# Performance work log

Hardware: AMD Instinct MI355X
Metric: run time of the kernel (lower is better)

Reference implementation:

```python
import jax, jax.numpy as jnp
import numpy as np

B, OUT_LEN, IN_LEN, H = 8, 1024, 4096, 256


def setup_inputs() -> dict:
    key = jax.random.key(0)
    k1, k2, k3 = jax.random.split(key, 3)
    output = jax.random.normal(k1, (B, OUT_LEN, H), dtype=jnp.float32)
    encoder_outputs = jax.random.normal(k2, (B, IN_LEN, H), dtype=jnp.float32)
    # valid lengths in [1, IN_LEN] so every softmax row has >=1 unmasked entry
    lengths = jax.random.randint(k3, (B,), 1, IN_LEN + 1).astype(jnp.int32)
    return {"output": output, "encoder_outputs": encoder_outputs, "lengths": lengths}


def reference(output, encoder_outputs, lengths):
    # scores: [B, out_len, in_len], unscaled dot-product (as in the original)
    scores = jnp.einsum('boh,bih->boi', output, encoder_outputs)
    # mask[b, j] = j < lengths[b]; masked positions get -inf (additive mask)
    valid = jnp.arange(encoder_outputs.shape[1])[None, :] < lengths[:, None]  # [B, in_len]
    scores = jnp.where(valid[:, None, :], scores, -jnp.inf)
    attn = jax.nn.softmax(scores, axis=-1)  # [B, out_len, in_len]
    context = jnp.einsum('boi,bih->boh', attn, encoder_outputs)  # [B, out_len, H]
    return (context, attn)
```

## Files before the change

kernel.cpp:

```cpp
#include <hip/hip_runtime.h>
#include <hip/hip_bf16.h>
#include <math.h>

#define B_    8
#define OLEN  1024
#define ILEN  4096
#define HDIM  256
#define LDA   40
#define KSPLIT 4

typedef __attribute__((ext_vector_type(8))) short bf16x8;
typedef __attribute__((ext_vector_type(4))) float f32x4;

__device__ inline unsigned pk_bf16(float x, float y) {
  union { __hip_bfloat162 h; unsigned u; } c;
  c.h = __float22bfloat162_rn(make_float2(x, y));
  return c.u;
}
__device__ inline short f2bf(float x) {
  union { __hip_bfloat16 h; short s; } c;
  c.h = __float2bfloat16(x);
  return c.s;
}

struct HiLo { uint4 hi, lo; };
__device__ inline HiLo split8(const float* __restrict__ p) {
  float4 v0 = *(const float4*)p;
  float4 v1 = *(const float4*)(p + 4);
  float f[8] = {v0.x, v0.y, v0.z, v0.w, v1.x, v1.y, v1.z, v1.w};
  unsigned hu[8]; float lo[8];
#pragma unroll
  for (int i = 0; i < 8; ++i) {
    unsigned u = __float_as_uint(f[i]);
    hu[i] = u & 0xffff0000u;
    lo[i] = f[i] - __uint_as_float(hu[i]);
  }
  HiLo r;
  r.hi = make_uint4((hu[0] >> 16) | hu[1], (hu[2] >> 16) | hu[3],
                    (hu[4] >> 16) | hu[5], (hu[6] >> 16) | hu[7]);
  r.lo = make_uint4(pk_bf16(lo[0], lo[1]), pk_bf16(lo[2], lo[3]),
                    pk_bf16(lo[4], lo[5]), pk_bf16(lo[6], lo[7]));
  return r;
}

__device__ inline void gl_lds16(const void* g, void* l) {
  __builtin_amdgcn_global_load_lds(
      (const __attribute__((address_space(1))) unsigned*)g,
      (__attribute__((address_space(3))) unsigned*)(l), 16, 0, 0);
}

__global__ __launch_bounds__(256) void k_prep_q(const float* __restrict__ Q,
                                                short* __restrict__ Qhi,
                                                short* __restrict__ Qlo) {
  const size_t idx = ((size_t)blockIdx.x * 256 + threadIdx.x) * 8;
  HiLo r = split8(&Q[idx]);
  *(uint4*)&Qhi[idx] = r.hi;
  *(uint4*)&Qlo[idx] = r.lo;
}

__global__ __launch_bounds__(256) void k_prep_e(const float* __restrict__ E,
                                                short* __restrict__ Ehi,
                                                short* __restrict__ Elo,
                                                short* __restrict__ ET,
                                                const int* __restrict__ len) {
  const int it = blockIdx.x, ht = blockIdx.y, b = blockIdx.z;
  const int L = len[b];
  const int t = threadIdx.x;
  if (it * 32 >= L) {
    const int h = t >> 3, i0 = (t & 7) * 4;
    *(uint2*)&ET[((size_t)(b * HDIM + ht * 32 + h)) * ILEN + it * 32 + i0] =
        make_uint2(0u, 0u);
    return;
  }
  __shared__ short Lsh[32][36];
  {
    const int i = t >> 3, h0 = (t & 7) * 4;
    const size_t gidx = ((size_t)(b * ILEN + it * 32 + i)) * HDIM + ht * 32 + h0;
    float4 v = *(const float4*)&E[gidx];
    float f[4] = {v.x, v.y, v.z, v.w};
    unsigned hs[4]; float lo[4];
#pragma unroll
    for (int j = 0; j < 4; ++j) {
      unsigned u = __float_as_uint(f[j]);
      hs[j] = u & 0xffff0000u;
      lo[j] = f[j] - __uint_as_float(hs[j]);
    }
    *(uint2*)&Ehi[gidx] = make_uint2((hs[0] >> 16) | hs[1], (hs[2] >> 16) | hs[3]);
    *(uint2*)&Elo[gidx] = make_uint2(pk_bf16(lo[0], lo[1]), pk_bf16(lo[2], lo[3]));
    Lsh[h0 + 0][i] = f2bf(f[0]);
    Lsh[h0 + 1][i] = f2bf(f[1]);
    Lsh[h0 + 2][i] = f2bf(f[2]);
    Lsh[h0 + 3][i] = f2bf(f[3]);
  }
  __syncthreads();
  {
    const int h = t >> 3, i0 = (t & 7) * 4;
    *(uint2*)&ET[((size_t)(b * HDIM + ht * 32 + h)) * ILEN + it * 32 + i0] =
        *(const uint2*)&Lsh[h][i0];
  }
}

__global__ __launch_bounds__(256) void k_scores_pre(
    const short* __restrict__ Qhi, const short* __restrict__ Qlo,
    const short* __restrict__ Ehi, const short* __restrict__ Elo,
    float* __restrict__ S, float2* __restrict__ stat,
    const int* __restrict__ len) {
  const int it = blockIdx.x, ot = blockIdx.y, b = blockIdx.z;
  const int L = len[b];
  if (it * 128 >= L) return;

  const size_t qoff = ((size_t)b * OLEN + ot * 128) * HDIM;
  const size_t eoff = ((size_t)b * ILEN + it * 128) * HDIM;

  __shared__ __align__(16) short Ah[128 * 32], Al[128 * 32];
  __shared__ __align__(16) short Bh[128 * 32], Bl[128 * 32];

  const int t = threadIdx.x;
  const int w = t >> 6, l = t & 63;
  const int la = l & 15, quad = l >> 4;
  const int mw = (w & 1) * 64, nw = (w >> 1) * 64;

  int sgoff[2], sloff[2];
#pragma unroll
  for (int j = 0; j < 2; ++j) {
    const int row = (w * 2 + j) * 16 + (l >> 2);
    const int c = (l & 3) ^ ((row >> 1) & 3);
    sgoff[j] = row * HDIM + c * 8;
    sloff[j] = ((w * 2 + j) * 64 + l) * 8;
  }

  f32x4 acc[4][4] = {};

  for (int kc = 0; kc < HDIM; kc += 32) {
#pragma unroll
    for (int j = 0; j < 2; ++j) {
      const size_t ga = qoff + sgoff[j] + kc;
      const size_t gb = eoff + sgoff[j] + kc;
      gl_lds16(&Qhi[ga], &Ah[sloff[j]]);
      gl_lds16(&Qlo[ga], &Al[sloff[j]]);
      gl_lds16(&Ehi[gb], &Bh[sloff[j]]);
      gl_lds16(&Elo[gb], &Bl[sloff[j]]);
    }
    __syncthreads();
    bf16x8 ah[4], al[4];
#pragma unroll
    for (int mi = 0; mi < 4; ++mi) {
      const int row = mw + mi * 16 + la;
      const int off = row * 32 + (quad ^ ((row >> 1) & 3)) * 8;
      ah[mi] = *(const bf16x8*)&Ah[off];
      al[mi] = *(const bf16x8*)&Al[off];
    }
#pragma unroll
    for (int ni = 0; ni < 4; ++ni) {
      const int row = nw + ni * 16 + la;
      const int off = row * 32 + (quad ^ ((row >> 1) & 3)) * 8;
      bf16x8 bh = *(const bf16x8*)&Bh[off];
      bf16x8 bl = *(const bf16x8*)&Bl[off];
#pragma unroll
      for (int mi = 0; mi < 4; ++mi) {
        acc[mi][ni] = __builtin_amdgcn_mfma_f32_16x16x32_bf16(ah[mi], bh, acc[mi][ni], 0, 0, 0);
        acc[mi][ni] = __builtin_amdgcn_mfma_f32_16x16x32_bf16(ah[mi], bl, acc[mi][ni], 0, 0, 0);
        acc[mi][ni] = __builtin_amdgcn_mfma_f32_16x16x32_bf16(al[mi], bh, acc[mi][ni], 0, 0, 0);
      }
    }
    __syncthreads();
  }

  float* Sb = S + ((size_t)b * OLEN + ot * 128) * (size_t)ILEN + it * 128;
#pragma unroll
  for (int mi = 0; mi < 4; ++mi)
#pragma unroll
    for (int ni = 0; ni < 4; ++ni)
#pragma unroll
      for (int r = 0; r < 4; ++r)
        Sb[(size_t)(mw + mi * 16 + quad * 4 + r) * ILEN + nw + ni * 16 + la] =
            acc[mi][ni][r];

  float* SM = (float*)Ah;
  float* SS = SM + 256;
  const int colbase = it * 128 + nw;

  float rmax[4][4];
#pragma unroll
  for (int mi = 0; mi < 4; ++mi)
#pragma unroll
    for (int r = 0; r < 4; ++r) {
      float mx = -INFINITY;
#pragma unroll
      for (int ni = 0; ni < 4; ++ni)
        if (colbase + ni * 16 + la < L) mx = fmaxf(mx, acc[mi][ni][r]);
      rmax[mi][r] = mx;
    }
#pragma unroll
  for (int o = 1; o < 16; o <<= 1)
#pragma unroll
    for (int mi = 0; mi < 4; ++mi)
#pragma unroll
      for (int r = 0; r < 4; ++r)
        rmax[mi][r] = fmaxf(rmax[mi][r], __shfl_xor(rmax[mi][r], o, 64));
  if (la == 0) {
#pragma unroll
    for (int mi = 0; mi < 4; ++mi)
#pragma unroll
      for (int r = 0; r < 4; ++r)
        SM[(w >> 1) * 128 + mw + mi * 16 + quad * 4 + r] = rmax[mi][r];
  }
  __syncthreads();

  float rsum[4][4];
#pragma unroll
  for (int mi = 0; mi < 4; ++mi)
#pragma unroll
    for (int r = 0; r < 4; ++r) {
      const int row = mw + mi * 16 + quad * 4 + r;
      const float M = fmaxf(SM[row], SM[128 + row]);
      float s = 0.f;
#pragma unroll
      for (int ni = 0; ni < 4; ++ni)
        if (colbase + ni * 16 + la < L) s += __expf(acc[mi][ni][r] - M);
      rsum[mi][r] = s;
    }
#pragma unroll
  for (int o = 1; o < 16; o <<= 1)
#pragma unroll
    for (int mi = 0; mi < 4; ++mi)
#pragma unroll
      for (int r = 0; r < 4; ++r)
        rsum[mi][r] += __shfl_xor(rsum[mi][r], o, 64);
  if (la == 0) {
#pragma unroll
    for (int mi = 0; mi < 4; ++mi)
#pragma unroll
      for (int r = 0; r < 4; ++r)
        SS[(w >> 1) * 128 + mw + mi * 16 + quad * 4 + r] = rsum[mi][r];
  }
  __syncthreads();

  if (t < 128) {
    const float m = fmaxf(SM[t], SM[128 + t]);
    const float s = SS[t] + SS[128 + t];
    stat[(size_t)it * (B_ * OLEN) + (size_t)b * OLEN + ot * 128 + t] =
        make_float2(m, s);
  }
}

__global__ __launch_bounds__(128) void k_combine(const float2* __restrict__ stat,
                                                 float2* __restrict__ rowstat,
                                                 const int* __restrict__ len) {
  const int row = blockIdx.x * 128 + threadIdx.x;
  const int b = row >> 10;
  const int nt = (len[b] + 127) >> 7;
  float2 v[32];
#pragma unroll
  for (int it = 0; it < 32; ++it)
    v[it] = stat[(size_t)it * (B_ * OLEN) + row];
  float m = -INFINITY;
#pragma unroll
  for (int it = 0; it < 32; ++it)
    if (it < nt) m = fmaxf(m, v[it].x);
  float s = 0.f;
#pragma unroll
  for (int it = 0; it < 32; ++it)
    if (it < nt) s += v[it].y * __expf(v[it].x - m);
  rowstat[row] = make_float2(m, 1.f / s);
}

__global__ __launch_bounds__(256) void k_context_fused(
    float* __restrict__ P, const short* __restrict__ ET,
    float* __restrict__ Cpart, const float2* __restrict__ rowstat,
    const int* __restrict__ len) {
  const int ot = blockIdx.x, ks = blockIdx.y, b = blockIdx.z;
  const int NC = ILEN / KSPLIT;
  float* Pb = P + ((size_t)b * OLEN + ot * 32) * (size_t)ILEN + ks * NC;
  const short* Tb = ET + (size_t)b * HDIM * ILEN + ks * NC;
  const int L = len[b];

  __shared__ __align__(16) short As[32 * 64];
  __shared__ __align__(16) short Bs[256 * 64];

  const int t = threadIdx.x;
  const int w = t >> 6, l = t & 63;
  const int la = l & 15, quad = l >> 4;
  const int mw = (w & 1) * 16, nw = (w >> 1) * 128;

  const int tr = t >> 3, tc = t & 7;
  const float2 st = rowstat[(size_t)b * OLEN + ot * 32 + tr];
  const float rm = st.x, rinv = st.y;

  int bslot[8];
#pragma unroll
  for (int j = 0; j < 8; ++j) bslot[j] = w * 512 + j * 64 + l;

  f32x4 acc[8] = {};

  const int rem = L - ks * NC;
  const int nv = rem <= 0 ? 0 : (rem >= NC ? NC / 64 : (rem + 63) >> 6);

  for (int ic = nv * 64; ic < NC; ic += 64) {
    float* arow = &Pb[(size_t)tr * ILEN + ic + tc * 8];
    const float4 z = make_float4(0.f, 0.f, 0.f, 0.f);
    *(float4*)(arow + 0) = z;
    *(float4*)(arow + 4) = z;
  }

  for (int c = 0; c < nv; ++c) {
    const int ic = c * 64;
#pragma unroll
    for (int j = 0; j < 8; ++j) {
      const int s = bslot[j];
      const int row = s >> 3, pc = s & 7;
      const int cc = pc ^ (row & 7);
      gl_lds16(&Tb[(size_t)row * ILEN + ic + cc * 8], &Bs[s * 8]);
    }
    {
      float* arow = &Pb[(size_t)tr * ILEN + ic + tc * 8];
      float4 g0 = *(const float4*)(arow + 0);
      float4 g1 = *(const float4*)(arow + 4);
      float v[8] = {g0.x, g0.y, g0.z, g0.w, g1.x, g1.y, g1.z, g1.w};
      const int i0 = ks * NC + ic + tc * 8;
#pragma unroll
      for (int j = 0; j < 8; ++j)
        v[j] = (i0 + j < L) ? __expf(v[j] - rm) * rinv : 0.f;
      *(float4*)(arow + 0) = make_float4(v[0], v[1], v[2], v[3]);
      *(float4*)(arow + 4) = make_float4(v[4], v[5], v[6], v[7]);
      uint4 w0 = make_uint4(pk_bf16(v[0], v[1]), pk_bf16(v[2], v[3]),
                            pk_bf16(v[4], v[5]), pk_bf16(v[6], v[7]));
      *(uint4*)&As[tr * 64 + (tc ^ (tr & 7)) * 8] = w0;
    }
    __syncthreads();
#pragma unroll
    for (int ki = 0; ki < 2; ++ki) {
      const int arow = mw + la;
      bf16x8 af = *(const bf16x8*)&As[arow * 64 + ((ki * 4 + quad) ^ (arow & 7)) * 8];
#pragma unroll
      for (int ni = 0; ni < 8; ++ni) {
        const int row = nw + ni * 16 + la;
        bf16x8 bfr = *(const bf16x8*)&Bs[row * 64 + ((ki * 4 + quad) ^ (row & 7)) * 8];
        acc[ni] = __builtin_amdgcn_mfma_f32_16x16x32_bf16(af, bfr, acc[ni], 0, 0, 0);
      }
    }
    __syncthreads();
  }

  float* Cb = Cpart + (size_t)ks * (B_ * OLEN * HDIM) +
              ((size_t)b * OLEN + ot * 32) * HDIM;
#pragma unroll
  for (int ni = 0; ni < 8; ++ni)
#pragma unroll
    for (int r = 0; r < 4; ++r)
      Cb[(size_t)(mw + quad * 4 + r) * HDIM + nw + ni * 16 + la] = acc[ni][r];
}

__global__ __launch_bounds__(256) void k_reduce(const float* __restrict__ Cp,
                                                float* __restrict__ ctx) {
  const size_t idx = ((size_t)blockIdx.x * 256 + threadIdx.x) * 8;
  const size_t n = (size_t)B_ * OLEN * HDIM;
  float a[8];
  {
    float4 a0 = *(const float4*)&Cp[idx];
    float4 a1 = *(const float4*)&Cp[idx + 4];
    a[0] = a0.x; a[1] = a0.y; a[2] = a0.z; a[3] = a0.w;
    a[4] = a1.x; a[5] = a1.y; a[6] = a1.z; a[7] = a1.w;
  }
#pragma unroll
  for (int k = 1; k < KSPLIT; ++k) {
    float4 b0 = *(const float4*)&Cp[(size_t)k * n + idx];
    float4 b1 = *(const float4*)&Cp[(size_t)k * n + idx + 4];
    a[0] += b0.x; a[1] += b0.y; a[2] += b0.z; a[3] += b0.w;
    a[4] += b1.x; a[5] += b1.y; a[6] += b1.z; a[7] += b1.w;
  }
  *(float4*)&ctx[idx]     = make_float4(a[0], a[1], a[2], a[3]);
  *(float4*)&ctx[idx + 4] = make_float4(a[4], a[5], a[6], a[7]);
}

__global__ __launch_bounds__(256) void k_softmax(float* __restrict__ A,
                                                 const int* __restrict__ len) {
  const int row = blockIdx.x;
  const int b   = row >> 10;
  const int L   = len[b];
  float* p = A + (size_t)row * ILEN;
  const int t = threadIdx.x;

  float v[16];
#pragma unroll
  for (int k = 0; k < 4; ++k) {
    float4 x = *(const float4*)&p[4 * t + 1024 * k];
    v[4 * k + 0] = x.x; v[4 * k + 1] = x.y;
    v[4 * k + 2] = x.z; v[4 * k + 3] = x.w;
  }
  float m = -INFINITY;
#pragma unroll
  for (int k = 0; k < 4; ++k)
#pragma unroll
    for (int j = 0; j < 4; ++j) {
      const int i = 4 * t + 1024 * k + j;
      if (i < L) m = fmaxf(m, v[4 * k + j]);
    }
  for (int o = 32; o > 0; o >>= 1) m = fmaxf(m, __shfl_xor(m, o, 64));
  __shared__ float sm[4], ss[4];
  const int w = t >> 6;
  if ((t & 63) == 0) sm[w] = m;
  __syncthreads();
  m = fmaxf(fmaxf(sm[0], sm[1]), fmaxf(sm[2], sm[3]));
  float s = 0.f;
#pragma unroll
  for (int k = 0; k < 4; ++k)
#pragma unroll
    for (int j = 0; j < 4; ++j) {
      const int i = 4 * t + 1024 * k + j;
      float pv = (i < L) ? __expf(v[4 * k + j] - m) : 0.f;
      v[4 * k + j] = pv;
      s += pv;
    }
  for (int o = 32; o > 0; o >>= 1) s += __shfl_xor(s, o, 64);
  if ((t & 63) == 0) ss[w] = s;
  __syncthreads();
  s = ss[0] + ss[1] + ss[2] + ss[3];
  const float inv = 1.f / s;
#pragma unroll
  for (int k = 0; k < 4; ++k) {
    float4 x = make_float4(v[4 * k + 0] * inv, v[4 * k + 1] * inv,
                           v[4 * k + 2] * inv, v[4 * k + 3] * inv);
    *(float4*)&p[4 * t + 1024 * k] = x;
  }
}

__global__ __launch_bounds__(256) void k_etrans(const float* __restrict__ E,
                                                short* __restrict__ ET) {
  const int it = blockIdx.x, ht = blockIdx.y, b = blockIdx.z;
  __shared__ short Lsh[32][36];
  const int t = threadIdx.x;
  {
    const int i = t >> 3, h0 = (t & 7) * 4;
    float4 v = *(const float4*)&E[((size_t)(b * ILEN + it * 32 + i)) * HDIM + ht * 32 + h0];
    Lsh[h0 + 0][i] = f2bf(v.x);
    Lsh[h0 + 1][i] = f2bf(v.y);
    Lsh[h0 + 2][i] = f2bf(v.z);
    Lsh[h0 + 3][i] = f2bf(v.w);
  }
  __syncthreads();
  {
    const int h = t >> 3, i0 = (t & 7) * 4;
    *(uint2*)&ET[((size_t)(b * HDIM + ht * 32 + h)) * ILEN + it * 32 + i0] =
        *(const uint2*)&Lsh[h][i0];
  }
}

__global__ __launch_bounds__(256) void k_scores_split(const float* __restrict__ Q,
                                                      const float* __restrict__ E,
                                                      float* __restrict__ S) {
  const int b = blockIdx.z, ot = blockIdx.y, it = blockIdx.x;
  const float* Qb = Q + ((size_t)b * OLEN + ot * 64) * HDIM;
  const float* Eb = E + ((size_t)b * ILEN + it * 64) * HDIM;

  __shared__ __align__(16) short Ah[64 * LDA], Al[64 * LDA];
  __shared__ __align__(16) short Bh[64 * LDA], Bl[64 * LDA];

  const int t = threadIdx.x;
  const int w = t >> 6, l = t & 63;
  const int la = l & 15, quad = l >> 4;
  const int sr = t >> 2, sc = (t & 3) * 8;

  f32x4 acc[4] = {};

#pragma unroll
  for (int kc = 0; kc < HDIM; kc += 32) {
    HiLo qa = split8(&Qb[(size_t)sr * HDIM + kc + sc]);
    HiLo eb = split8(&Eb[(size_t)sr * HDIM + kc + sc]);
    *(uint4*)&Ah[sr * LDA + sc] = qa.hi;
    *(uint4*)&Al[sr * LDA + sc] = qa.lo;
    *(uint4*)&Bh[sr * LDA + sc] = eb.hi;
    *(uint4*)&Bl[sr * LDA + sc] = eb.lo;
    __syncthreads();
    bf16x8 ah = *(const bf16x8*)&Ah[(w * 16 + la) * LDA + quad * 8];
    bf16x8 al = *(const bf16x8*)&Al[(w * 16 + la) * LDA + quad * 8];
#pragma unroll
    for (int n = 0; n < 4; ++n) {
      bf16x8 bh = *(const bf16x8*)&Bh[(n * 16 + la) * LDA + quad * 8];
      bf16x8 bl = *(const bf16x8*)&Bl[(n * 16 + la) * LDA + quad * 8];
      acc[n] = __builtin_amdgcn_mfma_f32_16x16x32_bf16(ah, bh, acc[n], 0, 0, 0);
      acc[n] = __builtin_amdgcn_mfma_f32_16x16x32_bf16(ah, bl, acc[n], 0, 0, 0);
      acc[n] = __builtin_amdgcn_mfma_f32_16x16x32_bf16(al, bh, acc[n], 0, 0, 0);
    }
    __syncthreads();
  }

  float* Sb = S + ((size_t)b * OLEN + ot * 64) * (size_t)ILEN + it * 64;
#pragma unroll
  for (int n = 0; n < 4; ++n)
#pragma unroll
    for (int r = 0; r < 4; ++r)
      Sb[(size_t)(w * 16 + quad * 4 + r) * ILEN + n * 16 + la] = acc[n][r];
}

__global__ __launch_bounds__(256) void k_context_f32(const float* __restrict__ P,
                                                     const short* __restrict__ ET,
                                                     float* __restrict__ C) {
  const int ot = blockIdx.x, ht = blockIdx.y, b = blockIdx.z;
  const float* Pb = P + ((size_t)b * OLEN + ot * 64) * (size_t)ILEN;
  const short* Tb = ET + ((size_t)b * HDIM + ht * 64) * (size_t)ILEN;

  __shared__ __align__(16) short As[64 * LDA], Bs[64 * LDA];

  const int t = threadIdx.x;
  const int w = t >> 6, l = t & 63;
  const int la = l & 15, quad = l >> 4;
  const int sr = t >> 2, sc = (t & 3) * 8;

  f32x4 acc[4] = {};

  for (int ic = 0; ic < ILEN; ic += 32) {
    {
      float4 p0 = *(const float4*)&Pb[(size_t)sr * ILEN + ic + sc];
      float4 p1 = *(const float4*)&Pb[(size_t)sr * ILEN + ic + sc + 4];
      uint4 aw = make_uint4(pk_bf16(p0.x, p0.y), pk_bf16(p0.z, p0.w),
                            pk_bf16(p1.x, p1.y), pk_bf16(p1.z, p1.w));
      *(uint4*)&As[sr * LDA + sc] = aw;
      uint4 bw = *(const uint4*)&Tb[(size_t)sr * ILEN + ic + sc];
      *(uint4*)&Bs[sr * LDA + sc] = bw;
    }
    __syncthreads();
    bf16x8 a = *(const bf16x8*)&As[(w * 16 + la) * LDA + quad * 8];
#pragma unroll
    for (int n = 0; n < 4; ++n) {
      bf16x8 bb = *(const bf16x8*)&Bs[(n * 16 + la) * LDA + quad * 8];
      acc[n] = __builtin_amdgcn_mfma_f32_16x16x32_bf16(a, bb, acc[n], 0, 0, 0);
    }
    __syncthreads();
  }

  float* Cb = C + ((size_t)b * OLEN + ot * 64) * HDIM + ht * 64;
#pragma unroll
  for (int n = 0; n < 4; ++n)
#pragma unroll
    for (int r = 0; r < 4; ++r)
      Cb[(size_t)(w * 16 + quad * 4 + r) * HDIM + n * 16 + la] = acc[n][r];
}

extern "C" void kernel_launch(void* const* d_in, const int* in_sizes, int n_in,
                              void* d_out, int out_size, void* d_ws, size_t ws_size,
                              hipStream_t stream) {
  (void)in_sizes; (void)n_in; (void)out_size;
  const float* outp = (const float*)d_in[0];
  const float* enc  = (const float*)d_in[1];
  const int*   len  = (const int*)d_in[2];

  float* ctx  = (float*)d_out;
  float* attn = ctx + (size_t)B_ * OLEN * HDIM;

  short* ws = (short*)d_ws;
  const size_t M = 1024 * 1024;
  short* ET = ws;

  if (ws_size >= 56ull * 1024 * 1024) {
    short* Qhi = ws + 8 * M;
    short* Qlo = ws + 10 * M;
    short* Ehi = ws + 12 * M;
    short* Elo = ws + 20 * M;
    float* Cpart = (float*)(ws + 8 * M);
    float2* stat = (float2*)ctx;
    float2* rowstat = stat + (size_t)(ILEN / 128) * B_ * OLEN;

    k_prep_q<<<(B_ * OLEN * HDIM) / (256 * 8), 256, 0, stream>>>(outp, Qhi, Qlo);
    dim3 gp(ILEN / 32, HDIM / 32, B_);
    k_prep_e<<<gp, 256, 0, stream>>>(enc, Ehi, Elo, ET, len);
    dim3 g1(ILEN / 128, OLEN / 128, B_);
    k_scores_pre<<<g1, 256, 0, stream>>>(Qhi, Qlo, Ehi, Elo, attn, stat, len);
    k_combine<<<(B_ * OLEN) / 128, 128, 0, stream>>>(stat, rowstat, len);
    dim3 g3(OLEN / 32, KSPLIT, B_);
    k_context_fused<<<g3, 256, 0, stream>>>(attn, ET, Cpart, rowstat, len);
    k_reduce<<<(B_ * OLEN * HDIM) / (256 * 8), 256, 0, stream>>>(Cpart, ctx);
  } else {
    dim3 gt(ILEN / 32, HDIM / 32, B_);
    k_etrans<<<gt, 32 * 8, 0, stream>>>(enc, ET);
    k_scores_split<<<dim3(ILEN / 64, OLEN / 64, B_), 256, 0, stream>>>(outp, enc, attn);
    k_softmax<<<B_ * OLEN, 256, 0, stream>>>(attn, len);
    dim3 g3(OLEN / 64, HDIM / 64, B_);
    k_context_f32<<<g3, 256, 0, stream>>>(attn, ET, ctx);
  }
}
```

Before: 304.8 us.

## Drop LDS staging in context kernel, load operands directly into registers

```diff
diff --git a/kernel.cpp b/kernel.cpp
--- a/kernel.cpp
+++ b/kernel.cpp
@@ -271,84 +271,75 @@
     const int* __restrict__ len) {
   const int ot = blockIdx.x, ks = blockIdx.y, b = blockIdx.z;
   const int NC = ILEN / KSPLIT;
-  float* Pb = P + ((size_t)b * OLEN + ot * 32) * (size_t)ILEN + ks * NC;
+  float* Pb = P + ((size_t)b * OLEN + ot * 64) * (size_t)ILEN + ks * NC;
   const short* Tb = ET + (size_t)b * HDIM * ILEN + ks * NC;
   const int L = len[b];
 
-  __shared__ __align__(16) short As[32 * 64];
-  __shared__ __align__(16) short Bs[256 * 64];
-
   const int t = threadIdx.x;
   const int w = t >> 6, l = t & 63;
   const int la = l & 15, quad = l >> 4;
-  const int mw = (w & 1) * 16, nw = (w >> 1) * 128;
-
-  const int tr = t >> 3, tc = t & 7;
-  const float2 st = rowstat[(size_t)b * OLEN + ot * 32 + tr];
+  const int mw = w * 16;
+
+  const int arow = mw + la;
+  const float2 st = rowstat[(size_t)b * OLEN + ot * 64 + arow];
   const float rm = st.x, rinv = st.y;
 
-  int bslot[8];
-#pragma unroll
-  for (int j = 0; j < 8; ++j) bslot[j] = w * 512 + j * 64 + l;
-
-  f32x4 acc[8] = {};
+  f32x4 acc[16] = {};
 
   const int rem = L - ks * NC;
   const int nv = rem <= 0 ? 0 : (rem >= NC ? NC / 64 : (rem + 63) >> 6);
 
-  for (int ic = nv * 64; ic < NC; ic += 64) {
-    float* arow = &Pb[(size_t)tr * ILEN + ic + tc * 8];
+  {
     const float4 z = make_float4(0.f, 0.f, 0.f, 0.f);
-    *(float4*)(arow + 0) = z;
-    *(float4*)(arow + 4) = z;
+    for (int ic = nv * 64; ic < NC; ic += 64) {
+#pragma unroll
+      for (int ki = 0; ki < 2; ++ki) {
+        float* dst = &Pb[(size_t)arow * ILEN + ic + (ki * 4 + quad) * 8];
+        *(float4*)(dst + 0) = z;
+        *(float4*)(dst + 4) = z;
+      }
+    }
   }
 
   for (int c = 0; c < nv; ++c) {
     const int ic = c * 64;
-#pragma unroll
-    for (int j = 0; j < 8; ++j) {
-      const int s = bslot[j];
-      const int row = s >> 3, pc = s & 7;
-      const int cc = pc ^ (row & 7);
-      gl_lds16(&Tb[(size_t)row * ILEN + ic + cc * 8], &Bs[s * 8]);
-    }
-    {
-      float* arow = &Pb[(size_t)tr * ILEN + ic + tc * 8];
-      float4 g0 = *(const float4*)(arow + 0);
-      float4 g1 = *(const float4*)(arow + 4);
+    bf16x8 af[2];
+#pragma unroll
+    for (int ki = 0; ki < 2; ++ki) {
+      float* src = &Pb[(size_t)arow * ILEN + ic + (ki * 4 + quad) * 8];
+      float4 g0 = *(const float4*)(src + 0);
+      float4 g1 = *(const float4*)(src + 4);
       float v[8] = {g0.x, g0.y, g0.z, g0.w, g1.x, g1.y, g1.z, g1.w};
-      const int i0 = ks * NC + ic + tc * 8;
+      const int i0 = ks * NC + ic + (ki * 4 + quad) * 8;
 #pragma unroll
       for (int j = 0; j < 8; ++j)
         v[j] = (i0 + j < L) ? __expf(v[j] - rm) * rinv : 0.f;
-      *(float4*)(arow + 0) = make_float4(v[0], v[1], v[2], v[3]);
-      *(float4*)(arow + 4) = make_float4(v[4], v[5], v[6], v[7]);
-      uint4 w0 = make_uint4(pk_bf16(v[0], v[1]), pk_bf16(v[2], v[3]),
+      *(float4*)(src + 0) = make_float4(v[0], v[1], v[2], v[3]);
+      *(float4*)(src + 4) = make_float4(v[4], v[5], v[6], v[7]);
+      uint4 pk = make_uint4(pk_bf16(v[0], v[1]), pk_bf16(v[2], v[3]),
                             pk_bf16(v[4], v[5]), pk_bf16(v[6], v[7]));
-      *(uint4*)&As[tr * 64 + (tc ^ (tr & 7)) * 8] = w0;
-    }
-    __syncthreads();
-#pragma unroll
-    for (int ki = 0; ki < 2; ++ki) {
-      const int arow = mw + la;
-      bf16x8 af = *(const bf16x8*)&As[arow * 64 + ((ki * 4 + quad) ^ (arow & 7)) * 8];
-#pragma unroll
-      for (int ni = 0; ni < 8; ++ni) {
-        const int row = nw + ni * 16 + la;
-        bf16x8 bfr = *(const bf16x8*)&Bs[row * 64 + ((ki * 4 + quad) ^ (row & 7)) * 8];
-        acc[ni] = __builtin_amdgcn_mfma_f32_16x16x32_bf16(af, bfr, acc[ni], 0, 0, 0);
+      union { uint4 u; bf16x8 h; } cv;
+      cv.u = pk;
+      af[ki] = cv.h;
+    }
+#pragma unroll
+    for (int ki = 0; ki < 2; ++ki)
+#pragma unroll
+      for (int ni = 0; ni < 16; ++ni) {
+        const int hrow = ni * 16 + la;
+        bf16x8 bfr =
+            *(const bf16x8*)&Tb[(size_t)hrow * ILEN + ic + (ki * 4 + quad) * 8];
+        acc[ni] = __builtin_amdgcn_mfma_f32_16x16x32_bf16(af[ki], bfr, acc[ni], 0, 0, 0);
       }
-    }
-    __syncthreads();
   }
 
   float* Cb = Cpart + (size_t)ks * (B_ * OLEN * HDIM) +
-              ((size_t)b * OLEN + ot * 32) * HDIM;
-#pragma unroll
-  for (int ni = 0; ni < 8; ++ni)
+              ((size_t)b * OLEN + ot * 64) * HDIM;
+#pragma unroll
+  for (int ni = 0; ni < 16; ++ni)
 #pragma unroll
     for (int r = 0; r < 4; ++r)
-      Cb[(size_t)(mw + quad * 4 + r) * HDIM + nw + ni * 16 + la] = acc[ni][r];
+      Cb[(size_t)(mw + quad * 4 + r) * HDIM + ni * 16 + la] = acc[ni][r];
 }
 
 __global__ __launch_bounds__(256) void k_reduce(const float* __restrict__ Cp,
@@ -567,12 +558,12 @@
     dim3 g1(ILEN / 128, OLEN / 128, B_);
     k_scores_pre<<<g1, 256, 0, stream>>>(Qhi, Qlo, Ehi, Elo, attn, stat, len);
     k_combine<<<(B_ * OLEN) / 128, 128, 0, stream>>>(stat, rowstat, len);
-    dim3 g3(OLEN / 32, KSPLIT, B_);
+    dim3 g3(OLEN / 64, KSPLIT, B_);
     k_context_fused<<<g3, 256, 0, stream>>>(attn, ET, Cpart, rowstat, len);
     k_reduce<<<(B_ * OLEN * HDIM) / (256 * 8), 256, 0, stream>>>(Cpart, ctx);
   } else {
     dim3 gt(ILEN / 32, HDIM / 32, B_);
-    k_etrans<<<gt, 32 * 8, 0, stream>>>(enc, ET);
+    k_etrans<<<gt, 256, 0, stream>>>(enc, ET);
     k_scores_split<<<dim3(ILEN / 64, OLEN / 64, B_), 256, 0, stream>>>(outp, enc, attn);
     k_softmax<<<B_ * OLEN, 256, 0, stream>>>(attn, len);
     dim3 g3(OLEN / 64, HDIM / 64, B_);
```

New measurement: 403.3 us. 32.3% more time.

## Fuse prep kernels, store exp in scores, fold row-stat combine into context kernel

Applied to the files above, without the earlier changes.

```diff
diff --git a/kernel.cpp b/kernel.cpp
--- a/kernel.cpp
+++ b/kernel.cpp
@@ -49,23 +49,25 @@
       (__attribute__((address_space(3))) unsigned*)(l), 16, 0, 0);
 }
 
-__global__ __launch_bounds__(256) void k_prep_q(const float* __restrict__ Q,
-                                                short* __restrict__ Qhi,
-                                                short* __restrict__ Qlo) {
-  const size_t idx = ((size_t)blockIdx.x * 256 + threadIdx.x) * 8;
-  HiLo r = split8(&Q[idx]);
-  *(uint4*)&Qhi[idx] = r.hi;
-  *(uint4*)&Qlo[idx] = r.lo;
-}
-
-__global__ __launch_bounds__(256) void k_prep_e(const float* __restrict__ E,
-                                                short* __restrict__ Ehi,
-                                                short* __restrict__ Elo,
-                                                short* __restrict__ ET,
-                                                const int* __restrict__ len) {
+__global__ __launch_bounds__(256) void k_prep(const float* __restrict__ Q,
+                                              const float* __restrict__ E,
+                                              short* __restrict__ Qhi,
+                                              short* __restrict__ Qlo,
+                                              short* __restrict__ Ehi,
+                                              short* __restrict__ Elo,
+                                              short* __restrict__ ET,
+                                              const int* __restrict__ len) {
+  const int t = threadIdx.x;
+  if (blockIdx.y == 8) {
+    const int flat = blockIdx.z * 128 + blockIdx.x;
+    const size_t idx = (size_t)flat * 2048 + t * 8;
+    HiLo r = split8(&Q[idx]);
+    *(uint4*)&Qhi[idx] = r.hi;
+    *(uint4*)&Qlo[idx] = r.lo;
+    return;
+  }
   const int it = blockIdx.x, ht = blockIdx.y, b = blockIdx.z;
   const int L = len[b];
-  const int t = threadIdx.x;
   if (it * 32 >= L) {
     const int h = t >> 3, i0 = (t & 7) * 4;
     *(uint2*)&ET[((size_t)(b * HDIM + ht * 32 + h)) * ILEN + it * 32 + i0] =
@@ -166,16 +168,6 @@
     __syncthreads();
   }
 
-  float* Sb = S + ((size_t)b * OLEN + ot * 128) * (size_t)ILEN + it * 128;
-#pragma unroll
-  for (int mi = 0; mi < 4; ++mi)
-#pragma unroll
-    for (int ni = 0; ni < 4; ++ni)
-#pragma unroll
-      for (int r = 0; r < 4; ++r)
-        Sb[(size_t)(mw + mi * 16 + quad * 4 + r) * ILEN + nw + ni * 16 + la] =
-            acc[mi][ni][r];
-
   float* SM = (float*)Ah;
   float* SS = SM + 256;
   const int colbase = it * 128 + nw;
@@ -207,6 +199,7 @@
   }
   __syncthreads();
 
+  float* Sb = S + ((size_t)b * OLEN + ot * 128) * (size_t)ILEN + it * 128;
   float rsum[4][4];
 #pragma unroll
   for (int mi = 0; mi < 4; ++mi)
@@ -216,8 +209,11 @@
       const float M = fmaxf(SM[row], SM[128 + row]);
       float s = 0.f;
 #pragma unroll
-      for (int ni = 0; ni < 4; ++ni)
-        if (colbase + ni * 16 + la < L) s += __expf(acc[mi][ni][r] - M);
+      for (int ni = 0; ni < 4; ++ni) {
+        const float p = __expf(acc[mi][ni][r] - M);
+        Sb[(size_t)row * ILEN + nw + ni * 16 + la] = p;
+        if (colbase + ni * 16 + la < L) s += p;
+      }
       rsum[mi][r] = s;
     }
 #pragma unroll
@@ -244,30 +240,9 @@
   }
 }
 
-__global__ __launch_bounds__(128) void k_combine(const float2* __restrict__ stat,
-                                                 float2* __restrict__ rowstat,
-                                                 const int* __restrict__ len) {
-  const int row = blockIdx.x * 128 + threadIdx.x;
-  const int b = row >> 10;
-  const int nt = (len[b] + 127) >> 7;
-  float2 v[32];
-#pragma unroll
-  for (int it = 0; it < 32; ++it)
-    v[it] = stat[(size_t)it * (B_ * OLEN) + row];
-  float m = -INFINITY;
-#pragma unroll
-  for (int it = 0; it < 32; ++it)
-    if (it < nt) m = fmaxf(m, v[it].x);
-  float s = 0.f;
-#pragma unroll
-  for (int it = 0; it < 32; ++it)
-    if (it < nt) s += v[it].y * __expf(v[it].x - m);
-  rowstat[row] = make_float2(m, 1.f / s);
-}
-
 __global__ __launch_bounds__(256) void k_context_fused(
     float* __restrict__ P, const short* __restrict__ ET,
-    float* __restrict__ Cpart, const float2* __restrict__ rowstat,
+    float* __restrict__ Cpart, const float2* __restrict__ stat,
     const int* __restrict__ len) {
   const int ot = blockIdx.x, ks = blockIdx.y, b = blockIdx.z;
   const int NC = ILEN / KSPLIT;
@@ -277,15 +252,40 @@
 
   __shared__ __align__(16) short As[32 * 64];
   __shared__ __align__(16) short Bs[256 * 64];
+  __shared__ float ssc[32][8];
 
   const int t = threadIdx.x;
   const int w = t >> 6, l = t & 63;
   const int la = l & 15, quad = l >> 4;
   const int mw = (w & 1) * 16, nw = (w >> 1) * 128;
-
   const int tr = t >> 3, tc = t & 7;
-  const float2 st = rowstat[(size_t)b * OLEN + ot * 32 + tr];
-  const float rm = st.x, rinv = st.y;
+
+  {
+    const int rowg = b * OLEN + ot * 32 + tr;
+    const int nt = (L + 127) >> 7;
+    float2 v0 = stat[(size_t)(tc + 0)  * (B_ * OLEN) + rowg];
+    float2 v1 = stat[(size_t)(tc + 8)  * (B_ * OLEN) + rowg];
+    float2 v2 = stat[(size_t)(tc + 16) * (B_ * OLEN) + rowg];
+    float2 v3 = stat[(size_t)(tc + 24) * (B_ * OLEN) + rowg];
+    float m = -INFINITY;
+    if (tc + 0  < nt) m = fmaxf(m, v0.x);
+    if (tc + 8  < nt) m = fmaxf(m, v1.x);
+    if (tc + 16 < nt) m = fmaxf(m, v2.x);
+    if (tc + 24 < nt) m = fmaxf(m, v3.x);
+#pragma unroll
+    for (int o = 1; o < 8; o <<= 1) m = fmaxf(m, __shfl_xor(m, o, 64));
+    float s = 0.f;
+    if (tc + 0  < nt) s += v0.y * __expf(v0.x - m);
+    if (tc + 8  < nt) s += v1.y * __expf(v1.x - m);
+    if (tc + 16 < nt) s += v2.y * __expf(v2.x - m);
+    if (tc + 24 < nt) s += v3.y * __expf(v3.x - m);
+#pragma unroll
+    for (int o = 1; o < 8; o <<= 1) s += __shfl_xor(s, o, 64);
+    const float inv = 1.f / s;
+    float2 vt = (ks == 0) ? v0 : (ks == 1) ? v1 : (ks == 2) ? v2 : v3;
+    ssc[tr][tc] = __expf(vt.x - m) * inv;
+  }
+  __syncthreads();
 
   int bslot[8];
 #pragma unroll
@@ -316,11 +316,12 @@
       float* arow = &Pb[(size_t)tr * ILEN + ic + tc * 8];
       float4 g0 = *(const float4*)(arow + 0);
       float4 g1 = *(const float4*)(arow + 4);
+      const float sc = ssc[tr][c >> 1];
       float v[8] = {g0.x, g0.y, g0.z, g0.w, g1.x, g1.y, g1.z, g1.w};
       const int i0 = ks * NC + ic + tc * 8;
 #pragma unroll
       for (int j = 0; j < 8; ++j)
-        v[j] = (i0 + j < L) ? __expf(v[j] - rm) * rinv : 0.f;
+        v[j] = (i0 + j < L) ? v[j] * sc : 0.f;
       *(float4*)(arow + 0) = make_float4(v[0], v[1], v[2], v[3]);
       *(float4*)(arow + 4) = make_float4(v[4], v[5], v[6], v[7]);
       uint4 w0 = make_uint4(pk_bf16(v[0], v[1]), pk_bf16(v[2], v[3]),
@@ -559,20 +560,17 @@
     short* Elo = ws + 20 * M;
     float* Cpart = (float*)(ws + 8 * M);
     float2* stat = (float2*)ctx;
-    float2* rowstat = stat + (size_t)(ILEN / 128) * B_ * OLEN;
-
-    k_prep_q<<<(B_ * OLEN * HDIM) / (256 * 8), 256, 0, stream>>>(outp, Qhi, Qlo);
-    dim3 gp(ILEN / 32, HDIM / 32, B_);
-    k_prep_e<<<gp, 256, 0, stream>>>(enc, Ehi, Elo, ET, len);
+
+    k_prep<<<dim3(ILEN / 32, 9, B_), 256, 0, stream>>>(outp, enc, Qhi, Qlo,
+                                                       Ehi, Elo, ET, len);
     dim3 g1(ILEN / 128, OLEN / 128, B_);
     k_scores_pre<<<g1, 256, 0, stream>>>(Qhi, Qlo, Ehi, Elo, attn, stat, len);
-    k_combine<<<(B_ * OLEN) / 128, 128, 0, stream>>>(stat, rowstat, len);
     dim3 g3(OLEN / 32, KSPLIT, B_);
-    k_context_fused<<<g3, 256, 0, stream>>>(attn, ET, Cpart, rowstat, len);
+    k_context_fused<<<g3, 256, 0, stream>>>(attn, ET, Cpart, stat, len);
     k_reduce<<<(B_ * OLEN * HDIM) / (256 * 8), 256, 0, stream>>>(Cpart, ctx);
   } else {
     dim3 gt(ILEN / 32, HDIM / 32, B_);
-    k_etrans<<<gt, 32 * 8, 0, stream>>>(enc, ET);
+    k_etrans<<<gt, 256, 0, stream>>>(enc, ET);
     k_scores_split<<<dim3(ILEN / 64, OLEN / 64, B_), 256, 0, stream>>>(outp, enc, attn);
     k_softmax<<<B_ * OLEN, 256, 0, stream>>>(attn, len);
     dim3 g3(OLEN / 64, HDIM / 64, B_);
```

Result: no change. 299.1 us (-1.9%).
